# Performance work log

Hardware: AMD Instinct MI355X
Metric: run time of the kernel (lower is better)

Reference implementation:

```python
import jax, jax.numpy as jnp
import numpy as np

MAX_VAL = 1000000000000.0


def setup_inputs() -> dict:
    key = jax.random.key(0)
    k1, k2, k3, k4 = jax.random.split(key, 4)
    B, H, N, D = 2, 16, 2048, 64
    query = jax.random.normal(k1, (B, H, N, D), dtype=jnp.float32)
    key_t = jax.random.normal(k2, (B, H, N, D), dtype=jnp.float32)
    value = jax.random.normal(k3, (B, H, N, D), dtype=jnp.float32)
    mask = jax.random.randint(k4, (B, 1, 1, N), 0, 2).astype(bool)
    return {"query": query, "key": key_t, "value": value, "mask": mask,
            "global_num": 8, "window_size": 64}


def reference(query, key, value, mask, global_num, window_size):
    # query/key/value: [B, H, N, D]; mask: [B, 1, 1, N] bool (True = keep)
    B, H, N, D = query.shape
    scale = 1.0 / jnp.sqrt(jnp.asarray(D, dtype=query.dtype))

    # split heads: first global_num are global, rest are local (windowed)
    q_g, k_g, v_g = query[:, :global_num], key[:, :global_num], value[:, :global_num]
    q_l, k_l, v_l = query[:, global_num:], key[:, global_num:], value[:, global_num:]

    # ---- global heads: dense masked attention ----
    scores_g = jnp.einsum('bhqd,bhkd->bhqk', q_g, k_g) * scale
    scores_g = jnp.where(mask, scores_g, -MAX_VAL)
    p_g = jax.nn.softmax(scores_g, axis=-1)
    out_g = jnp.einsum('bhqk,bhkd->bhqd', p_g, v_l[:, :0]) if False else jnp.einsum('bhqk,bhkd->bhqd', p_g, v_g)

    # ---- local heads: window-banded mask on top of padding mask ----
    pos = jnp.arange(N)
    distance = jnp.abs(pos[None, :] - pos[:, None])  # [N, N]
    band = (distance <= window_size)                 # [N, N] bool
    mask_l = mask & band                             # [B, 1, N, N]
    scores_l = jnp.einsum('bhqd,bhkd->bhqk', q_l, k_l) * scale
    scores_l = jnp.where(mask_l, scores_l, -MAX_VAL)
    p_l = jax.nn.softmax(scores_l, axis=-1)
    out_l = jnp.einsum('bhqk,bhkd->bhqd', p_l, v_l)

    out = jnp.concatenate([out_g, out_l], axis=1)  # [B, H, N, D]
    return (out, p_g, p_l)
```

## Files before the change

kernel.cpp:

```cpp
#include <hip/hip_runtime.h>
#include <stdint.h>

typedef __attribute__((ext_vector_type(8))) __bf16 bf16x8;
typedef __attribute__((ext_vector_type(4))) float f32x4;
typedef __attribute__((ext_vector_type(4))) int i32x4;

#define DEVI static __device__ __forceinline__

constexpr int NN = 2048;
constexpr int DD = 64;
constexpr int NH = 16;
constexpr int NG = 8;
constexpr float SCALE = 0.125f;
constexpr float NEGBIG = -1.0e12f;
constexpr size_t OUT_ELEMS = (size_t)2 * NH * NN * DD;
constexpr size_t PG_ELEMS  = (size_t)2 * NG * NN * NN;

struct Frag { bf16x8 hi, lo; };

DEVI Frag make_frag(const float* p) {
  f32x4 a = *(const f32x4*)p;
  f32x4 b = *(const f32x4*)(p + 4);
  Frag f;
#pragma unroll
  for (int j = 0; j < 8; j++) {
    float x = (j < 4) ? a[j] : b[j - 4];
    __bf16 h = (__bf16)x;
    f.hi[j] = h;
    f.lo[j] = (__bf16)(x - (float)h);
  }
  return f;
}

DEVI f32x4 mfma(bf16x8 a, bf16x8 b, f32x4 c) {
  return __builtin_amdgcn_mfma_f32_16x16x32_bf16(a, b, c, 0, 0, 0);
}

DEVI void compute_st(const Frag kf[2][2], const Frag* qf_rs, f32x4 acc[2]) {
#pragma unroll
  for (int Mt = 0; Mt < 2; Mt++) {
    f32x4 c = {0.f, 0.f, 0.f, 0.f};
#pragma unroll
    for (int ks = 0; ks < 2; ks++) {
      c = mfma(kf[Mt][ks].hi, qf_rs[ks].hi, c);
      c = mfma(kf[Mt][ks].hi, qf_rs[ks].lo, c);
      c = mfma(kf[Mt][ks].lo, qf_rs[ks].hi, c);
    }
    acc[Mt] = c;
  }
}

__global__ __launch_bounds__(256, 2)
void wattn(const float* __restrict__ Q, const float* __restrict__ K,
           const float* __restrict__ V, const int* __restrict__ MSK,
           float* __restrict__ OUT) {
  const int bid = blockIdx.x;
  const bool loc = bid >= 256;
  const int lb = loc ? bid - 256 : bid;
  const int bh = lb >> 4;
  const int b  = bh >> 3;
  const int hh = bh & 7;
  const int h  = loc ? (hh + 8) : hh;
  const int wave = (int)(threadIdx.x >> 6);
  const int lane = (int)(threadIdx.x & 63);
  const int qi = lane >> 4;
  const int li = lane & 15;
  const int rb = (lb & 15) * 128 + wave * 32;

  const float* qp = Q + ((size_t)(b * NH + h) * NN) * DD;
  const float* kp = K + ((size_t)(b * NH + h) * NN) * DD;
  const float* vp = V + ((size_t)(b * NH + h) * NN) * DD;
  const int*   mp = MSK + (size_t)b * NN;
  float* op = OUT + ((size_t)(b * NH + h) * NN) * DD;
  float* pp = OUT + OUT_ELEMS + (loc ? PG_ELEMS : (size_t)0)
                  + ((size_t)(b * NG + hh) * NN) * NN;

  Frag qf[2][2];
#pragma unroll
  for (int rs = 0; rs < 2; rs++)
#pragma unroll
    for (int ks = 0; ks < 2; ks++)
      qf[rs][ks] = make_frag(qp + (size_t)(rb + rs * 16 + li) * DD + ks * 32 + qi * 8);

  int wlo = 0, whi = 0;
  if (loc) {
    wlo = rb - 64; if (wlo < 0) wlo = 0;
    whi = rb + 96; if (whi > NN) whi = NN;
    const f32x4 z = {0.f, 0.f, 0.f, 0.f};
#pragma unroll 1
    for (int rr = 0; rr < 32; rr++) {
      float* dst = pp + (size_t)(rb + rr) * NN;
#pragma unroll 1
      for (int c = lane * 4; c < NN; c += 256) {
        if (c >= wlo && c < whi) continue;
        *(f32x4*)(dst + c) = z;
      }
    }
  }

  const int ntiles = loc ? 5 : 64;

  float m[2] = {NEGBIG, NEGBIG};
  float l[2] = {0.f, 0.f};

#pragma unroll 1
  for (int t = 0; t < ntiles; t++) {
    const int wc = loc ? (rb - 64 + 32 * t) : (32 * t);
    if (wc < 0 || wc >= NN) continue;

    Frag kf[2][2];
#pragma unroll
    for (int Mt = 0; Mt < 2; Mt++)
#pragma unroll
      for (int ks = 0; ks < 2; ks++)
        kf[Mt][ks] = make_frag(kp + (size_t)(wc + Mt * 16 + li) * DD + ks * 32 + qi * 8);

    i32x4 mv[2];
    mv[0] = *(const i32x4*)(mp + wc + qi * 4);
    mv[1] = *(const i32x4*)(mp + wc + 16 + qi * 4);

#pragma unroll
    for (int rs = 0; rs < 2; rs++) {
      f32x4 acc[2];
      compute_st(kf, qf[rs], acc);
      const int row = rb + rs * 16 + li;
      float vals[8];
#pragma unroll
      for (int Mt = 0; Mt < 2; Mt++)
#pragma unroll
        for (int r = 0; r < 4; r++) {
          const int col = wc + Mt * 16 + qi * 4 + r;
          bool ok = (mv[Mt][r] != 0);
          if (loc) { int d = row - col; if (d < 0) d = -d; ok = ok && (d <= 64); }
          vals[Mt * 4 + r] = ok ? acc[Mt][r] * SCALE : NEGBIG;
        }
      float mx = vals[0];
#pragma unroll
      for (int j = 1; j < 8; j++) mx = fmaxf(mx, vals[j]);
      const float mn = fmaxf(m[rs], mx);
      float s = 0.f;
#pragma unroll
      for (int j = 0; j < 8; j++) s += __expf(vals[j] - mn);
      l[rs] = l[rs] * __expf(m[rs] - mn) + s;
      m[rs] = mn;
    }
  }

  float rl[2];
#pragma unroll
  for (int rs = 0; rs < 2; rs++) {
#pragma unroll
    for (int off = 16; off <= 32; off <<= 1) {
      const float mo = __shfl_xor(m[rs], off);
      const float lo2 = __shfl_xor(l[rs], off);
      const float mn = fmaxf(m[rs], mo);
      l[rs] = l[rs] * __expf(m[rs] - mn) + lo2 * __expf(mo - mn);
      m[rs] = mn;
    }
    rl[rs] = 1.0f / l[rs];
  }

  f32x4 o[2][4];
#pragma unroll
  for (int rs = 0; rs < 2; rs++)
#pragma unroll
    for (int dt = 0; dt < 4; dt++) o[rs][dt] = (f32x4){0.f, 0.f, 0.f, 0.f};

  const int srcA = (((qi * 2) + 0) & 3) * 16 + li;
  const int srcB = (((qi * 2) + 1) & 3) * 16 + li;
  const bool selB = (qi >> 1) != 0;

#pragma unroll 1
  for (int t = 0; t < ntiles; t++) {
    const int wc = loc ? (rb - 64 + 32 * t) : (32 * t);
    if (wc < 0 || wc >= NN) continue;

    Frag kf[2][2];
#pragma unroll
    for (int Mt = 0; Mt < 2; Mt++)
#pragma unroll
      for (int ks = 0; ks < 2; ks++)
        kf[Mt][ks] = make_frag(kp + (size_t)(wc + Mt * 16 + li) * DD + ks * 32 + qi * 8);

    i32x4 mv[2];
    mv[0] = *(const i32x4*)(mp + wc + qi * 4);
    mv[1] = *(const i32x4*)(mp + wc + 16 + qi * 4);

    bf16x8 vf[4];
#pragma unroll
    for (int dt = 0; dt < 4; dt++)
#pragma unroll
      for (int j = 0; j < 8; j++)
        vf[dt][j] = (__bf16)vp[(size_t)(wc + qi * 8 + j) * DD + dt * 16 + li];

#pragma unroll
    for (int rs = 0; rs < 2; rs++) {
      f32x4 acc[2];
      compute_st(kf, qf[rs], acc);
      const int row = rb + rs * 16 + li;
      float pf[8];
#pragma unroll
      for (int Mt = 0; Mt < 2; Mt++)
#pragma unroll
        for (int r = 0; r < 4; r++) {
          const int col = wc + Mt * 16 + qi * 4 + r;
          bool ok = (mv[Mt][r] != 0);
          if (loc) { int d = row - col; if (d < 0) d = -d; ok = ok && (d <= 64); }
          const float vv = ok ? acc[Mt][r] * SCALE : NEGBIG;
          pf[Mt * 4 + r] = __expf(vv - m[rs]) * rl[rs];
        }
      float pa[8];
#pragma unroll
      for (int j = 0; j < 8; j++) {
        const int src = (j < 4) ? srcA : srcB;
        const float v0 = __shfl(pf[0 + (j & 3)], src);
        const float v1 = __shfl(pf[4 + (j & 3)], src);
        pa[j] = selB ? v1 : v0;
      }
      float* prow = pp + (size_t)(rb + rs * 16 + li) * NN + wc + qi * 8;
      *(f32x4*)prow       = (f32x4){pa[0], pa[1], pa[2], pa[3]};
      *(f32x4*)(prow + 4) = (f32x4){pa[4], pa[5], pa[6], pa[7]};
      bf16x8 pb;
#pragma unroll
      for (int j = 0; j < 8; j++) pb[j] = (__bf16)pa[j];
#pragma unroll
      for (int dt = 0; dt < 4; dt++)
        o[rs][dt] = mfma(pb, vf[dt], o[rs][dt]);
    }
  }

#pragma unroll
  for (int rs = 0; rs < 2; rs++) {
#pragma unroll
    for (int dt = 0; dt < 4; dt++)
#pragma unroll
      for (int r = 0; r < 4; r++) {
        const int row = rb + rs * 16 + qi * 4 + r;
        op[(size_t)row * DD + dt * 16 + li] = o[rs][dt][r];
      }
  }
}

extern "C" void kernel_launch(void* const* d_in, const int* in_sizes, int n_in,
                              void* d_out, int out_size, void* d_ws, size_t ws_size,
                              hipStream_t stream) {
  (void)in_sizes; (void)n_in; (void)out_size; (void)d_ws; (void)ws_size;
  const float* Q = (const float*)d_in[0];
  const float* K = (const float*)d_in[1];
  const float* V = (const float*)d_in[2];
  const int*   M = (const int*)d_in[3];
  float* O = (float*)d_out;
  wattn<<<dim3(512), dim3(256), 0, stream>>>(Q, K, V, M, O);
}
```

Baseline: 745.5 us.

## Pre-split Q/K into bf16 hi/lo, transpose V, and drop softmax max tracking

Adds two pre-pass kernels. One writes bf16 hi/lo splits of Q and K into the workspace, and one writes a transposed bf16 copy of V. The attention kernel then loads ready-made MFMA fragments with vector loads instead of converting fp32 per tile, and it no longer does strided scalar V gathers. The softmax also drops the running-max rescaling and sums exp(score) weighted by the mask. This removes the max, shuffle-merge and extra exp work, but it can overflow for large scores and divides by zero for fully masked rows. The trade-off is the extra pre-pass traffic and launches, and the approach relies on score magnitudes staying small.

```diff
diff --git a/kernel.cpp b/kernel.cpp
--- a/kernel.cpp
+++ b/kernel.cpp
@@ -12,47 +12,69 @@
 constexpr int NH = 16;
 constexpr int NG = 8;
 constexpr float SCALE = 0.125f;
-constexpr float NEGBIG = -1.0e12f;
 constexpr size_t OUT_ELEMS = (size_t)2 * NH * NN * DD;
 constexpr size_t PG_ELEMS  = (size_t)2 * NG * NN * NN;
-
-struct Frag { bf16x8 hi, lo; };
-
-DEVI Frag make_frag(const float* p) {
-  f32x4 a = *(const f32x4*)p;
-  f32x4 b = *(const f32x4*)(p + 4);
-  Frag f;
+constexpr size_t E = (size_t)2 * NH * NN * DD;
+constexpr size_t QHI = 0, QLO = E, KHI = 2 * E, KLO = 3 * E, VTO = 4 * E;
+
+DEVI void split8(const float* __restrict__ src, __bf16* __restrict__ dhi,
+                 __bf16* __restrict__ dlo) {
+  f32x4 a = *(const f32x4*)src;
+  f32x4 b = *(const f32x4*)(src + 4);
+  bf16x8 hi, lo;
 #pragma unroll
   for (int j = 0; j < 8; j++) {
     float x = (j < 4) ? a[j] : b[j - 4];
     __bf16 h = (__bf16)x;
-    f.hi[j] = h;
-    f.lo[j] = (__bf16)(x - (float)h);
-  }
-  return f;
+    hi[j] = h;
+    lo[j] = (__bf16)(x - (float)h);
+  }
+  *(bf16x8*)dhi = hi;
+  *(bf16x8*)dlo = lo;
+}
+
+__global__ __launch_bounds__(256)
+void cvtqk(const float* __restrict__ Q, const float* __restrict__ K,
+           __bf16* __restrict__ W) {
+  const size_t o = ((size_t)blockIdx.x * 256 + threadIdx.x) * 8;
+  split8(Q + o, W + QHI + o, W + QLO + o);
+  split8(K + o, W + KHI + o, W + KLO + o);
+}
+
+__global__ __launch_bounds__(256)
+void vtrans(const float* __restrict__ V, __bf16* __restrict__ Vt) {
+  const size_t o = ((size_t)blockIdx.x * 256 + threadIdx.x) * 8;
+  const int n0 = (int)(o & (NN - 1));
+  const int d  = (int)((o >> 11) & 63);
+  const size_t bh = o >> 17;
+  const float* src = V + (bh << 17) + (size_t)n0 * DD + d;
+  bf16x8 v;
+#pragma unroll
+  for (int j = 0; j < 8; j++) v[j] = (__bf16)src[(size_t)j * DD];
+  *(bf16x8*)(Vt + o) = v;
 }
 
 DEVI f32x4 mfma(bf16x8 a, bf16x8 b, f32x4 c) {
   return __builtin_amdgcn_mfma_f32_16x16x32_bf16(a, b, c, 0, 0, 0);
 }
 
-DEVI void compute_st(const Frag kf[2][2], const Frag* qf_rs, f32x4 acc[2]) {
+DEVI void compute_st(const bf16x8 kh[2][2], const bf16x8 kl[2][2],
+                     const bf16x8 qh[2], const bf16x8 ql[2], f32x4 acc[2]) {
 #pragma unroll
   for (int Mt = 0; Mt < 2; Mt++) {
     f32x4 c = {0.f, 0.f, 0.f, 0.f};
 #pragma unroll
     for (int ks = 0; ks < 2; ks++) {
-      c = mfma(kf[Mt][ks].hi, qf_rs[ks].hi, c);
-      c = mfma(kf[Mt][ks].hi, qf_rs[ks].lo, c);
-      c = mfma(kf[Mt][ks].lo, qf_rs[ks].hi, c);
+      c = mfma(kh[Mt][ks], qh[ks], c);
+      c = mfma(kh[Mt][ks], ql[ks], c);
+      c = mfma(kl[Mt][ks], qh[ks], c);
     }
     acc[Mt] = c;
   }
 }
 
 __global__ __launch_bounds__(256, 2)
-void wattn(const float* __restrict__ Q, const float* __restrict__ K,
-           const float* __restrict__ V, const int* __restrict__ MSK,
+void wattn(const __bf16* __restrict__ W, const int* __restrict__ MSK,
            float* __restrict__ OUT) {
   const int bid = blockIdx.x;
   const bool loc = bid >= 256;
@@ -67,25 +89,30 @@
   const int li = lane & 15;
   const int rb = (lb & 15) * 128 + wave * 32;
 
-  const float* qp = Q + ((size_t)(b * NH + h) * NN) * DD;
-  const float* kp = K + ((size_t)(b * NH + h) * NN) * DD;
-  const float* vp = V + ((size_t)(b * NH + h) * NN) * DD;
+  const size_t hoff = ((size_t)(b * NH + h)) << 17;
+  const __bf16* qhp = W + QHI + hoff;
+  const __bf16* qlp = W + QLO + hoff;
+  const __bf16* khp = W + KHI + hoff;
+  const __bf16* klp = W + KLO + hoff;
+  const __bf16* vtp = W + VTO + hoff;
   const int*   mp = MSK + (size_t)b * NN;
-  float* op = OUT + ((size_t)(b * NH + h) * NN) * DD;
+  float* op = OUT + hoff;
   float* pp = OUT + OUT_ELEMS + (loc ? PG_ELEMS : (size_t)0)
                   + ((size_t)(b * NG + hh) * NN) * NN;
 
-  Frag qf[2][2];
+  bf16x8 qh[2][2], ql[2][2];
 #pragma unroll
   for (int rs = 0; rs < 2; rs++)
 #pragma unroll
-    for (int ks = 0; ks < 2; ks++)
-      qf[rs][ks] = make_frag(qp + (size_t)(rb + rs * 16 + li) * DD + ks * 32 + qi * 8);
-
-  int wlo = 0, whi = 0;
+    for (int ks = 0; ks < 2; ks++) {
+      const size_t off = (size_t)(rb + rs * 16 + li) * DD + ks * 32 + qi * 8;
+      qh[rs][ks] = *(const bf16x8*)(qhp + off);
+      ql[rs][ks] = *(const bf16x8*)(qlp + off);
+    }
+
   if (loc) {
-    wlo = rb - 64; if (wlo < 0) wlo = 0;
-    whi = rb + 96; if (whi > NN) whi = NN;
+    int wlo = rb - 64; if (wlo < 0) wlo = 0;
+    int whi = rb + 96; if (whi > NN) whi = NN;
     const f32x4 z = {0.f, 0.f, 0.f, 0.f};
 #pragma unroll 1
     for (int rr = 0; rr < 32; rr++) {
@@ -99,8 +126,6 @@
   }
 
   const int ntiles = loc ? 5 : 64;
-
-  float m[2] = {NEGBIG, NEGBIG};
   float l[2] = {0.f, 0.f};
 
 #pragma unroll 1
@@ -108,12 +133,15 @@
     const int wc = loc ? (rb - 64 + 32 * t) : (32 * t);
     if (wc < 0 || wc >= NN) continue;
 
-    Frag kf[2][2];
+    bf16x8 kh[2][2], kl[2][2];
 #pragma unroll
     for (int Mt = 0; Mt < 2; Mt++)
 #pragma unroll
-      for (int ks = 0; ks < 2; ks++)
-        kf[Mt][ks] = make_frag(kp + (size_t)(wc + Mt * 16 + li) * DD + ks * 32 + qi * 8);
+      for (int ks = 0; ks < 2; ks++) {
+        const size_t off = (size_t)(wc + Mt * 16 + li) * DD + ks * 32 + qi * 8;
+        kh[Mt][ks] = *(const bf16x8*)(khp + off);
+        kl[Mt][ks] = *(const bf16x8*)(klp + off);
+      }
 
     i32x4 mv[2];
     mv[0] = *(const i32x4*)(mp + wc + qi * 4);
@@ -122,9 +150,9 @@
 #pragma unroll
     for (int rs = 0; rs < 2; rs++) {
       f32x4 acc[2];
-      compute_st(kf, qf[rs], acc);
+      compute_st(kh, kl, qh[rs], ql[rs], acc);
       const int row = rb + rs * 16 + li;
-      float vals[8];
+      float s = 0.f;
 #pragma unroll
       for (int Mt = 0; Mt < 2; Mt++)
 #pragma unroll
@@ -132,31 +160,18 @@
           const int col = wc + Mt * 16 + qi * 4 + r;
           bool ok = (mv[Mt][r] != 0);
           if (loc) { int d = row - col; if (d < 0) d = -d; ok = ok && (d <= 64); }
-          vals[Mt * 4 + r] = ok ? acc[Mt][r] * SCALE : NEGBIG;
+          const float okf = ok ? 1.f : 0.f;
+          s += __expf(acc[Mt][r] * SCALE) * okf;
         }
-      float mx = vals[0];
-#pragma unroll
-      for (int j = 1; j < 8; j++) mx = fmaxf(mx, vals[j]);
-      const float mn = fmaxf(m[rs], mx);
-      float s = 0.f;
-#pragma unroll
-      for (int j = 0; j < 8; j++) s += __expf(vals[j] - mn);
-      l[rs] = l[rs] * __expf(m[rs] - mn) + s;
-      m[rs] = mn;
+      l[rs] += s;
     }
   }
 
   float rl[2];
 #pragma unroll
   for (int rs = 0; rs < 2; rs++) {
-#pragma unroll
-    for (int off = 16; off <= 32; off <<= 1) {
-      const float mo = __shfl_xor(m[rs], off);
-      const float lo2 = __shfl_xor(l[rs], off);
-      const float mn = fmaxf(m[rs], mo);
-      l[rs] = l[rs] * __expf(m[rs] - mn) + lo2 * __expf(mo - mn);
-      m[rs] = mn;
-    }
+    l[rs] += __shfl_xor(l[rs], 16);
+    l[rs] += __shfl_xor(l[rs], 32);
     rl[rs] = 1.0f / l[rs];
   }
 
@@ -175,28 +190,25 @@
     const int wc = loc ? (rb - 64 + 32 * t) : (32 * t);
     if (wc < 0 || wc >= NN) continue;
 
-    Frag kf[2][2];
+    bf16x8 kh[2][2], kl[2][2];
 #pragma unroll
     for (int Mt = 0; Mt < 2; Mt++)
 #pragma unroll
-      for (int ks = 0; ks < 2; ks++)
-        kf[Mt][ks] = make_frag(kp + (size_t)(wc + Mt * 16 + li) * DD + ks * 32 + qi * 8);
+      for (int ks = 0; ks < 2; ks++) {
+        const size_t off = (size_t)(wc + Mt * 16 + li) * DD + ks * 32 + qi * 8;
+        kh[Mt][ks] = *(const bf16x8*)(khp + off);
+        kl[Mt][ks] = *(const bf16x8*)(klp + off);
+      }
 
     i32x4 mv[2];
     mv[0] = *(const i32x4*)(mp + wc + qi * 4);
     mv[1] = *(const i32x4*)(mp + wc + 16 + qi * 4);
 
-    bf16x8 vf[4];
-#pragma unroll
-    for (int dt = 0; dt < 4; dt++)
-#pragma unroll
-      for (int j = 0; j < 8; j++)
-        vf[dt][j] = (__bf16)vp[(size_t)(wc + qi * 8 + j) * DD + dt * 16 + li];
-
+    bf16x8 pb[2];
 #pragma unroll
     for (int rs = 0; rs < 2; rs++) {
       f32x4 acc[2];
-      compute_st(kf, qf[rs], acc);
+      compute_st(kh, kl, qh[rs], ql[rs], acc);
       const int row = rb + rs * 16 + li;
       float pf[8];
 #pragma unroll
@@ -206,8 +218,8 @@
           const int col = wc + Mt * 16 + qi * 4 + r;
           bool ok = (mv[Mt][r] != 0);
           if (loc) { int d = row - col; if (d < 0) d = -d; ok = ok && (d <= 64); }
-          const float vv = ok ? acc[Mt][r] * SCALE : NEGBIG;
-          pf[Mt * 4 + r] = __expf(vv - m[rs]) * rl[rs];
+          const float okf = ok ? 1.f : 0.f;
+          pf[Mt * 4 + r] = __expf(acc[Mt][r] * SCALE) * okf * rl[rs];
         }
       float pa[8];
 #pragma unroll
@@ -220,17 +232,19 @@
       float* prow = pp + (size_t)(rb + rs * 16 + li) * NN + wc + qi * 8;
       *(f32x4*)prow       = (f32x4){pa[0], pa[1], pa[2], pa[3]};
       *(f32x4*)(prow + 4) = (f32x4){pa[4], pa[5], pa[6], pa[7]};
-      bf16x8 pb;
-#pragma unroll
-      for (int j = 0; j < 8; j++) pb[j] = (__bf16)pa[j];
-#pragma unroll
-      for (int dt = 0; dt < 4; dt++)
-        o[rs][dt] = mfma(pb, vf[dt], o[rs][dt]);
-    }
-  }
-
-#pragma unroll
-  for (int rs = 0; rs < 2; rs++) {
+#pragma unroll
+      for (int j = 0; j < 8; j++) pb[rs][j] = (__bf16)pa[j];
+    }
+#pragma unroll
+    for (int dt = 0; dt < 4; dt++) {
+      const bf16x8 vf = *(const bf16x8*)(vtp + (size_t)(dt * 16 + li) * NN + wc + qi * 8);
+      o[0][dt] = mfma(pb[0], vf, o[0][dt]);
+      o[1][dt] = mfma(pb[1], vf, o[1][dt]);
+    }
+  }
+
+#pragma unroll
+  for (int rs = 0; rs < 2; rs++)
 #pragma unroll
     for (int dt = 0; dt < 4; dt++)
 #pragma unroll
@@ -238,17 +252,20 @@
         const int row = rb + rs * 16 + qi * 4 + r;
         op[(size_t)row * DD + dt * 16 + li] = o[rs][dt][r];
       }
-  }
 }
 
 extern "C" void kernel_launch(void* const* d_in, const int* in_sizes, int n_in,
                               void* d_out, int out_size, void* d_ws, size_t ws_size,
                               hipStream_t stream) {
-  (void)in_sizes; (void)n_in; (void)out_size; (void)d_ws; (void)ws_size;
+  (void)in_sizes; (void)n_in; (void)out_size; (void)ws_size;
   const float* Q = (const float*)d_in[0];
   const float* K = (const float*)d_in[1];
   const float* V = (const float*)d_in[2];
   const int*   M = (const int*)d_in[3];
   float* O = (float*)d_out;
-  wattn<<<dim3(512), dim3(256), 0, stream>>>(Q, K, V, M, O);
-}
+  __bf16* W = (__bf16*)d_ws;
+  const int nblk = (int)(E / 8 / 256);
+  cvtqk<<<dim3(nblk), dim3(256), 0, stream>>>(Q, K, W);
+  vtrans<<<dim3(nblk), dim3(256), 0, stream>>>(V, W + VTO);
+  wattn<<<dim3(512), dim3(256), 0, stream>>>(W, M, O);
+}
```

New measurement: 791.5 us. +6.2%, slower.
